# Kernel optimization log

Hardware: AMD Instinct MI355X
Metric: run time of the kernel (lower is better)

Reference implementation:

```python
import jax, jax.numpy as jnp
import numpy as np

EPS = 1e-5

def _bn(x, g, b, m, v):
    # eval-mode batchnorm, NCHW, per-channel params
    inv = g / jnp.sqrt(v + EPS)
    return x * inv[None, :, None, None] + (b - m * inv)[None, :, None, None]

def setup_inputs() -> dict:
    key = jax.random.key(0)
    ks = jax.random.split(key, 16)
    C = 64
    x = jax.random.normal(ks[0], (8, C, 64, 64), dtype=jnp.float32)
    w1 = jax.random.normal(ks[1], (C, C, 1, 1), dtype=jnp.float32) * 0.1
    w2 = jax.random.normal(ks[2], (C, 1, 3, 3), dtype=jnp.float32) * 0.1
    w3 = jax.random.normal(ks[3], (C, C, 1, 1), dtype=jnp.float32) * 0.1
    def bn_params(k):
        k1, k2, k3, k4 = jax.random.split(k, 4)
        return (jax.random.uniform(k1, (C,)) + 0.5,
                jax.random.normal(k2, (C,)) * 0.1,
                jax.random.normal(k3, (C,)) * 0.1,
                jax.random.uniform(k4, (C,)) + 0.5)
    g1, b1, m1, v1 = bn_params(ks[4])
    g2, b2, m2, v2 = bn_params(ks[5])
    g3, b3, m3, v3 = bn_params(ks[6])
    return {"x": x, "w1": w1, "bn1_g": g1, "bn1_b": b1, "bn1_m": m1, "bn1_v": v1,
            "w2": w2, "bn2_g": g2, "bn2_b": b2, "bn2_m": m2, "bn2_v": v2,
            "w3": w3, "bn3_g": g3, "bn3_b": b3, "bn3_m": m3, "bn3_v": v3}

def reference(x, w1, bn1_g, bn1_b, bn1_m, bn1_v,
              w2, bn2_g, bn2_b, bn2_m, bn2_v,
              w3, bn3_g, bn3_b, bn3_m, bn3_v):
    B, c, h, w = x.shape
    N = h * w
    # conv1 (1x1) + BN + ReLU -> V
    v = jnp.einsum('bchw,oc->bohw', x, w1[:, :, 0, 0])
    v = jax.nn.relu(_bn(v, bn1_g, bn1_b, bn1_m, bn1_v))
    # attention over spatial positions: Q=K=x, single head, dim=c
    Q = x.reshape(B, c, N)          # bdn
    V = v.reshape(B, c, N)          # bdm
    scores = jnp.einsum('bdn,bdm->bnm', Q, Q) / (c ** 0.5)  # [B,N,N]
    prob = jax.nn.softmax(scores, axis=-1)
    out = jnp.einsum('bnm,bdm->bdn', prob, V).reshape(B, c, h, w)
    # depthwise conv + BN + ReLU
    out = jax.lax.conv_general_dilated(
        out, w2, window_strides=(1, 1), padding='SAME',
        dimension_numbers=('NCHW', 'OIHW', 'NCHW'), feature_group_count=c)
    out = jax.nn.relu(_bn(out, bn2_g, bn2_b, bn2_m, bn2_v))
    # pointwise conv + BN
    out = jnp.einsum('bchw,oc->bohw', out, w3[:, :, 0, 0])
    out = _bn(out, bn3_g, bn3_b, bn3_m, bn3_v)
    # residual (stride==1 and in_size==out_size)
    return out + x
```

## Files before the change

kernel.cpp:

```cpp
#include <hip/hip_runtime.h>
#include <stdint.h>

typedef __attribute__((ext_vector_type(8)))  short s16x8;
typedef __attribute__((ext_vector_type(16))) float f32x16;
typedef __attribute__((ext_vector_type(2)))  unsigned u32x2;

union CvtI4 { int4 i; s16x8 s; };
union CvtU4 { uint4 u; s16x8 s; };

__device__ __forceinline__ unsigned f2bf(float f) {
    union { float f; unsigned u; } v; v.f = f;
    return (v.u + 0x7fffu + ((v.u >> 16) & 1u)) >> 16;
}

__device__ __forceinline__ unsigned packbf(float lo, float hi) {
    union { float f; unsigned u; } a0, a1;
    a0.f = lo; a1.f = hi;
    return __builtin_amdgcn_perm(a1.u + 0x8000u, a0.u + 0x8000u, 0x07060302u);
}

__global__ __launch_bounds__(256) void k_prep(
    const float* __restrict__ x, const float* __restrict__ w1,
    const float* __restrict__ g1, const float* __restrict__ b1,
    const float* __restrict__ m1, const float* __restrict__ v1,
    unsigned short* __restrict__ xT, unsigned short* __restrict__ vbf)
{
    __shared__ float X[64 * 65];
    const int b    = blockIdx.x >> 7;
    const int n0   = ((blockIdx.x >> 1) & 63) << 6;
    const int half = blockIdx.x & 1;
    const int tid  = threadIdx.x;
    const float QS = 0.42466090014400953f;

    {
        const int r = tid >> 6, nn = tid & 63;
        const float* xb = x + (size_t)b * 262144 + n0 + nn;
#pragma unroll
        for (int cc = 0; cc < 16; ++cc) {
            int c = cc * 4 + r;
            X[c * 65 + nn] = xb[(size_t)c * 4096];
        }
    }
    __syncthreads();

    {
        const int n8 = tid >> 3, c8 = tid & 7;
        const int n = (half << 5) + n8;
        unsigned u[4];
#pragma unroll
        for (int j = 0; j < 4; ++j) {
            unsigned lo = f2bf(X[(c8 * 8 + 2 * j) * 65 + n] * QS);
            unsigned hi = f2bf(X[(c8 * 8 + 2 * j + 1) * 65 + n] * QS);
            u[j] = lo | (hi << 16);
        }
        uint4 pk; pk.x = u[0]; pk.y = u[1]; pk.z = u[2]; pk.w = u[3];
        *(uint4*)(xT + (((size_t)((b << 12) + n0 + n)) << 6) + (c8 << 3)) = pk;
    }

    {
        const int n = tid & 63, og = tid >> 6;
        float rX[64];
#pragma unroll
        for (int c = 0; c < 64; ++c) rX[c] = X[c * 65 + n];
        unsigned short* vb = vbf + (((size_t)(b << 6)) << 12) + n0 + n;
#pragma unroll 2
        for (int oo = 0; oo < 8; ++oo) {
            int o = (half << 5) + og * 8 + oo;
            float inv = g1[o] * rsqrtf(v1[o] + 1e-5f);
            float sh  = b1[o] - m1[o] * inv;
            float acc = 0.f;
#pragma unroll
            for (int c = 0; c < 64; ++c) acc = fmaf(w1[o * 64 + c], rX[c], acc);
            vb[(size_t)o << 12] = (unsigned short)f2bf(fmaxf(fmaf(acc, inv, sh), 0.f));
        }
    }
}

__global__ __launch_bounds__(512, 4) void k_attn(
    const unsigned short* __restrict__ xT, const unsigned short* __restrict__ vbf,
    unsigned short* __restrict__ outO)
{
    __shared__ __align__(16) unsigned short Kl[2][2][64 * 64];
    __shared__ __align__(16) unsigned short Vl[2][2][64 * 64];

    const int b    = blockIdx.x & 7;
    const int qgrp = blockIdx.x >> 3;
    const int tid  = threadIdx.x;
    const int w = tid >> 6, lane = tid & 63;
    const int l31 = lane & 31, half = lane >> 5;
    const int qbase = qgrp << 6;
    const int qd = w & 3, par = w >> 2;
    const int s = qd & 1;
    const int t = qd >> 1;

    s16x8 Bq[4];
    {
        const unsigned short* qr = xT +
            (((size_t)((b << 12) + qbase + (t << 5) + l31)) << 6) + (half << 3);
#pragma unroll
        for (int kk = 0; kk < 4; ++kk) {
            CvtI4 c; c.i = *(const int4*)(qr + (kk << 4));
            Bq[kk] = c.s;
        }
    }

    const int pt = tid >> 8;
    const int sr = (tid >> 3) & 31;
    const int sc = tid & 7;
    const unsigned short* kBase = xT  + ((size_t)b << 18) + (sr << 6) + (sc << 3);
    const unsigned short* vBase = vbf + ((size_t)b << 18) + ((size_t)sr << 12) + (sc << 3);
    const int kx  = (sc ^ (sr & 7)) << 3;
    const int d0  = (sr << 6) + kx;
    const int d1  = ((sr + 32) << 6) + kx;

    int4 kpA, kpB, vpA, vpB;

    {
        int4 a0 = *(const int4*)(kBase + ((size_t)pt << 12));
        int4 a1 = *(const int4*)(kBase + ((size_t)pt << 12) + (32 << 6));
        int4 b0 = *(const int4*)(vBase + (pt << 6));
        int4 b1v = *(const int4*)(vBase + ((size_t)32 << 12) + (pt << 6));
        unsigned short* Kd = &Kl[0][pt][0];
        unsigned short* Vd = &Vl[0][pt][0];
        *(int4*)(Kd + d0) = a0; *(int4*)(Kd + d1) = a1;
        *(int4*)(Vd + d0) = b0; *(int4*)(Vd + d1) = b1v;
        const int t1 = 2 + pt;
        kpA = *(const int4*)(kBase + ((size_t)t1 << 12));
        kpB = *(const int4*)(kBase + ((size_t)t1 << 12) + (32 << 6));
        vpA = *(const int4*)(vBase + (t1 << 6));
        vpB = *(const int4*)(vBase + ((size_t)32 << 12) + (t1 << 6));
    }
    __syncthreads();

    f32x16 O[2];
#pragma unroll
    for (int dl = 0; dl < 2; ++dl)
#pragma unroll
        for (int r = 0; r < 16; ++r) O[dl][r] = 0.f;
    float rs = 0.f;

    const int km = (s << 5) + l31;

    for (int p = 0; p < 32; ++p) {
        {
            unsigned short* Kd = &Kl[(p + 1) & 1][pt][0];
            unsigned short* Vd = &Vl[(p + 1) & 1][pt][0];
            *(int4*)(Kd + d0) = kpA; *(int4*)(Kd + d1) = kpB;
            *(int4*)(Vd + d0) = vpA; *(int4*)(Vd + d1) = vpB;
        }
        {
            int tn = ((p + 2) << 1) + pt; if (tn > 63) tn = 63;
            kpA = *(const int4*)(kBase + ((size_t)tn << 12));
            kpB = *(const int4*)(kBase + ((size_t)tn << 12) + (32 << 6));
            vpA = *(const int4*)(vBase + (tn << 6));
            vpB = *(const int4*)(vBase + ((size_t)32 << 12) + (tn << 6));
        }

        const unsigned short* Kb = &Kl[p & 1][par][0];
        s16x8 Ak[4];
#pragma unroll
        for (int kk = 0; kk < 4; ++kk)
            Ak[kk] = *(const s16x8*)(Kb + (km << 6) + ((((kk << 1) + half) ^ (km & 7)) << 3));
        f32x16 S = {0.f,0.f,0.f,0.f,0.f,0.f,0.f,0.f,0.f,0.f,0.f,0.f,0.f,0.f,0.f,0.f};
        __builtin_amdgcn_s_setprio(1);
        S = __builtin_amdgcn_mfma_f32_32x32x16_bf16(Ak[0], Bq[0], S, 0, 0, 0);
        S = __builtin_amdgcn_mfma_f32_32x32x16_bf16(Ak[1], Bq[1], S, 0, 0, 0);
        S = __builtin_amdgcn_mfma_f32_32x32x16_bf16(Ak[2], Bq[2], S, 0, 0, 0);
        S = __builtin_amdgcn_mfma_f32_32x32x16_bf16(Ak[3], Bq[3], S, 0, 0, 0);
        __builtin_amdgcn_s_setprio(0);

        uint2 G[4];
#pragma unroll
        for (int q = 0; q < 4; ++q) {
            float p0 = __builtin_amdgcn_exp2f(S[4*q+0]);
            float p1 = __builtin_amdgcn_exp2f(S[4*q+1]);
            float p2 = __builtin_amdgcn_exp2f(S[4*q+2]);
            float p3 = __builtin_amdgcn_exp2f(S[4*q+3]);
            rs += (p0 + p1) + (p2 + p3);
            G[q].x = packbf(p0, p1);
            G[q].y = packbf(p2, p3);
        }

        const unsigned short* Vb = &Vl[p & 1][par][0];
        __builtin_amdgcn_s_setprio(1);
#pragma unroll
        for (int ksl = 0; ksl < 2; ++ksl) {
            u32x2 r0 = __builtin_amdgcn_permlane32_swap(G[2*ksl].x, G[2*ksl+1].x, false, false);
            u32x2 r1 = __builtin_amdgcn_permlane32_swap(G[2*ksl].y, G[2*ksl+1].y, false, false);
            CvtU4 ac;
            ac.u.x = r0.x;
            ac.u.y = r1.x;
            ac.u.z = r0.y;
            ac.u.w = r1.y;
            const s16x8 Ap = ac.s;
#pragma unroll
            for (int dl = 0; dl < 2; ++dl) {
                const int drow = (dl << 5) + l31;
                const int cch = (s << 2) + (ksl << 1) + half;
                const s16x8 Bv = *(const s16x8*)(Vb + (drow << 6) + ((cch ^ (drow & 7)) << 3));
                O[dl] = __builtin_amdgcn_mfma_f32_32x32x16_bf16(Ap, Bv, O[dl], 0, 0, 0);
            }
        }
        __builtin_amdgcn_s_setprio(0);

        __syncthreads();
    }

    float* scr  = (float*)&Kl[0][0][0];
    float* scr2 = (float*)&Vl[0][0][0];
    float* rsL  = scr2 + 4096;
    float* dnm  = rsL + 256;

    rs += __shfl_xor(rs, 32);
    if (half == 0) rsL[(w << 5) + l31] = rs;
    if (par == 1) {
#pragma unroll
        for (int dl = 0; dl < 2; ++dl)
#pragma unroll
            for (int r = 0; r < 16; ++r)
                scr[((((qd << 1) + dl)) << 10) + (r << 6) + lane] = O[dl][r];
    }
    __syncthreads();

    if (tid < 64) {
        int tt = tid >> 5, n = tid & 31;
        dnm[tid] = (rsL[((tt << 1) << 5) + n] + rsL[(((tt << 1) + 1) << 5) + n]) +
                   (rsL[(((tt << 1) + 4) << 5) + n] + rsL[(((tt << 1) + 5) << 5) + n]);
    }
    if (par == 0) {
#pragma unroll
        for (int dl = 0; dl < 2; ++dl)
#pragma unroll
            for (int r = 0; r < 16; ++r)
                O[dl][r] += scr[((((qd << 1) + dl)) << 10) + (r << 6) + lane];
        if (s == 1) {
#pragma unroll
            for (int dl = 0; dl < 2; ++dl)
#pragma unroll
                for (int r = 0; r < 16; ++r)
                    scr2[((((t << 1) + dl)) << 10) + (r << 6) + lane] = O[dl][r];
        }
    }
    __syncthreads();

    if (par == 0 && s == 0) {
        const int nb = (b << 12) + qbase;
#pragma unroll
        for (int r = 0; r < 16; ++r) {
            int rowoff = (r & 3) + ((r >> 2) << 3) + (half << 2);
            int n = (t << 5) + rowoff;
            float inv = 1.f / dnm[n];
#pragma unroll
            for (int dl = 0; dl < 2; ++dl) {
                float o = O[dl][r] + scr2[((((t << 1) + dl)) << 10) + (r << 6) + lane];
                outO[((size_t)(nb + n) << 6) + (dl << 5) + l31] =
                    (unsigned short)f2bf(o * inv);
            }
        }
    }
}

__global__ __launch_bounds__(256) void k_post(
    const unsigned short* __restrict__ Obase,
    const float* __restrict__ x,
    const float* __restrict__ w2,
    const float* __restrict__ g2, const float* __restrict__ b2,
    const float* __restrict__ m2, const float* __restrict__ v2,
    const float* __restrict__ w3,
    const float* __restrict__ g3, const float* __restrict__ b3,
    const float* __restrict__ m3, const float* __restrict__ v3,
    float* __restrict__ out)
{
    __shared__ float W[3][34 * 66];
    __shared__ float T2[32 * 66];

    const int b  = blockIdx.x >> 7;
    const int h  = (blockIdx.x >> 1) & 63;
    const int wh = blockIdx.x & 1;
    const int wbase = wh << 5;
    const int tid = threadIdx.x;

#pragma unroll
    for (int r = 0; r < 3; ++r) {
        int hh = h + r - 1;
#pragma unroll
        for (int i = 0; i < 2; ++i) {
            int lin = (i << 8) + tid;
            if (lin < 272) {
                int wl = lin >> 3, cg = lin & 7;
                int wg = wbase + wl - 1;
                float* Wd = &W[r][wl * 66 + (cg << 3)];
                if (hh >= 0 && hh <= 63 && wg >= 0 && wg <= 63) {
                    size_t npos = (size_t)((b << 12) + (hh << 6) + wg);
                    uint4 v = *(const uint4*)(Obase + (npos << 6) + (cg << 3));
                    union { float f; unsigned u; } t;
                    t.u = v.x << 16;         Wd[0] = t.f;
                    t.u = v.x & 0xFFFF0000u; Wd[1] = t.f;
                    t.u = v.y << 16;         Wd[2] = t.f;
                    t.u = v.y & 0xFFFF0000u; Wd[3] = t.f;
                    t.u = v.z << 16;         Wd[4] = t.f;
                    t.u = v.z & 0xFFFF0000u; Wd[5] = t.f;
                    t.u = v.w << 16;         Wd[6] = t.f;
                    t.u = v.w & 0xFFFF0000u; Wd[7] = t.f;
                } else {
#pragma unroll
                    for (int j = 0; j < 8; ++j) Wd[j] = 0.f;
                }
            }
        }
    }
    __syncthreads();

    const int w32 = tid & 31, cq = tid >> 5;
    float t8[8];
#pragma unroll
    for (int i = 0; i < 8; ++i) t8[i] = 0.f;

#pragma unroll
    for (int ky = 0; ky < 3; ++ky) {
#pragma unroll
        for (int kx = 0; kx < 3; ++kx) {
            const int k = ky * 3 + kx;
            const float* Wr = &W[ky][(w32 + kx) * 66 + (cq << 3)];
#pragma unroll
            for (int i = 0; i < 2; ++i) {
                float4 a = *(const float4*)(Wr + (i << 2));
                int c = (cq << 3) + (i << 2);
                t8[i * 4 + 0] = fmaf(w2[(c + 0) * 9 + k], a.x, t8[i * 4 + 0]);
                t8[i * 4 + 1] = fmaf(w2[(c + 1) * 9 + k], a.y, t8[i * 4 + 1]);
                t8[i * 4 + 2] = fmaf(w2[(c + 2) * 9 + k], a.z, t8[i * 4 + 2]);
                t8[i * 4 + 3] = fmaf(w2[(c + 3) * 9 + k], a.w, t8[i * 4 + 3]);
            }
        }
    }
#pragma unroll
    for (int i = 0; i < 8; ++i) {
        int c = (cq << 3) + i;
        float inv = g2[c] * rsqrtf(v2[c] + 1e-5f);
        float sh  = b2[c] - m2[c] * inv;
        T2[w32 * 66 + c] = fmaxf(fmaf(t8[i], inv, sh), 0.f);
    }
    __syncthreads();

    float rT[64];
#pragma unroll
    for (int c4 = 0; c4 < 16; ++c4)
        *(float4*)&rT[c4 << 2] = *(const float4*)&T2[w32 * 66 + (c4 << 2)];

    const int hw = (h << 6) + wbase + w32;
#pragma unroll 2
    for (int oo = 0; oo < 8; ++oo) {
        int o = (cq << 3) + oo;
        float inv = g3[o] * rsqrtf(v3[o] + 1e-5f);
        float sh  = b3[o] - m3[o] * inv;
        float acc = 0.f;
#pragma unroll
        for (int c = 0; c < 64; ++c) acc = fmaf(w3[o * 64 + c], rT[c], acc);
        size_t idx = (((size_t)((b << 6) + o)) << 12) + hw;
        out[idx] = fmaf(acc, inv, sh) + x[idx];
    }
}

extern "C" void kernel_launch(void* const* d_in, const int* in_sizes, int n_in,
                              void* d_out, int out_size, void* d_ws, size_t ws_size,
                              hipStream_t stream)
{
    const float* x  = (const float*)d_in[0];
    const float* w1 = (const float*)d_in[1];
    const float* g1 = (const float*)d_in[2];
    const float* b1 = (const float*)d_in[3];
    const float* m1 = (const float*)d_in[4];
    const float* v1 = (const float*)d_in[5];
    const float* w2 = (const float*)d_in[6];
    const float* g2 = (const float*)d_in[7];
    const float* b2 = (const float*)d_in[8];
    const float* m2 = (const float*)d_in[9];
    const float* v2 = (const float*)d_in[10];
    const float* w3 = (const float*)d_in[11];
    const float* g3 = (const float*)d_in[12];
    const float* b3 = (const float*)d_in[13];
    const float* m3 = (const float*)d_in[14];
    const float* v3 = (const float*)d_in[15];
    float* out = (float*)d_out;

    unsigned short* xT  = (unsigned short*)d_ws;
    unsigned short* vbf = xT + (size_t)8 * 4096 * 64;
    unsigned short* Obase = (unsigned short*)((char*)d_ws + (8u << 20));

    k_prep<<<1024, 256, 0, stream>>>(x, w1, g1, b1, m1, v1, xT, vbf);
    k_attn<<<512, 512, 0, stream>>>(xT, vbf, Obase);
    k_post<<<1024, 256, 0, stream>>>(Obase, x, w2, g2, b2, m2, v2,
                                     w3, g3, b3, m3, v3, out);
}
```

Measured before the change: 184.8 us.

## Double query tile per attention block to reuse K/V tiles across two query groups

Result: no change. 184.7 us (-0.1%).

```diff
diff --git a/kernel.cpp b/kernel.cpp
--- a/kernel.cpp
+++ b/kernel.cpp
@@ -76,31 +76,34 @@
     }
 }
 
-__global__ __launch_bounds__(512, 4) void k_attn(
+__global__ __launch_bounds__(512, 2) void k_attn(
     const unsigned short* __restrict__ xT, const unsigned short* __restrict__ vbf,
     unsigned short* __restrict__ outO)
 {
     __shared__ __align__(16) unsigned short Kl[2][2][64 * 64];
     __shared__ __align__(16) unsigned short Vl[2][2][64 * 64];
-
-    const int b    = blockIdx.x & 7;
-    const int qgrp = blockIdx.x >> 3;
-    const int tid  = threadIdx.x;
+    __shared__ float rsL[8][2][32];
+    __shared__ float dnm[128];
+
+    const int b   = blockIdx.x & 7;
+    const int qg2 = blockIdx.x >> 3;
+    const int tid = threadIdx.x;
     const int w = tid >> 6, lane = tid & 63;
     const int l31 = lane & 31, half = lane >> 5;
-    const int qbase = qgrp << 6;
+    const int qbase = qg2 << 7;
     const int qd = w & 3, par = w >> 2;
     const int s = qd & 1;
     const int t = qd >> 1;
 
-    s16x8 Bq[4];
-    {
+    s16x8 Bq[2][4];
+#pragma unroll
+    for (int ti = 0; ti < 2; ++ti) {
         const unsigned short* qr = xT +
-            (((size_t)((b << 12) + qbase + (t << 5) + l31)) << 6) + (half << 3);
+            (((size_t)((b << 12) + qbase + ((t + 2 * ti) << 5) + l31)) << 6) + (half << 3);
 #pragma unroll
         for (int kk = 0; kk < 4; ++kk) {
             CvtI4 c; c.i = *(const int4*)(qr + (kk << 4));
-            Bq[kk] = c.s;
+            Bq[ti][kk] = c.s;
         }
     }
 
@@ -132,12 +135,14 @@
     }
     __syncthreads();
 
-    f32x16 O[2];
-#pragma unroll
-    for (int dl = 0; dl < 2; ++dl)
-#pragma unroll
-        for (int r = 0; r < 16; ++r) O[dl][r] = 0.f;
-    float rs = 0.f;
+    f32x16 O[2][2];
+#pragma unroll
+    for (int ti = 0; ti < 2; ++ti)
+#pragma unroll
+        for (int dl = 0; dl < 2; ++dl)
+#pragma unroll
+            for (int r = 0; r < 16; ++r) O[ti][dl][r] = 0.f;
+    float rs[2] = {0.f, 0.f};
 
     const int km = (s << 5) + l31;
 
@@ -161,44 +166,50 @@
 #pragma unroll
         for (int kk = 0; kk < 4; ++kk)
             Ak[kk] = *(const s16x8*)(Kb + (km << 6) + ((((kk << 1) + half) ^ (km & 7)) << 3));
-        f32x16 S = {0.f,0.f,0.f,0.f,0.f,0.f,0.f,0.f,0.f,0.f,0.f,0.f,0.f,0.f,0.f,0.f};
-        __builtin_amdgcn_s_setprio(1);
-        S = __builtin_amdgcn_mfma_f32_32x32x16_bf16(Ak[0], Bq[0], S, 0, 0, 0);
-        S = __builtin_amdgcn_mfma_f32_32x32x16_bf16(Ak[1], Bq[1], S, 0, 0, 0);
-        S = __builtin_amdgcn_mfma_f32_32x32x16_bf16(Ak[2], Bq[2], S, 0, 0, 0);
-        S = __builtin_amdgcn_mfma_f32_32x32x16_bf16(Ak[3], Bq[3], S, 0, 0, 0);
-        __builtin_amdgcn_s_setprio(0);
-
-        uint2 G[4];
-#pragma unroll
-        for (int q = 0; q < 4; ++q) {
-            float p0 = __builtin_amdgcn_exp2f(S[4*q+0]);
-            float p1 = __builtin_amdgcn_exp2f(S[4*q+1]);
-            float p2 = __builtin_amdgcn_exp2f(S[4*q+2]);
-            float p3 = __builtin_amdgcn_exp2f(S[4*q+3]);
-            rs += (p0 + p1) + (p2 + p3);
-            G[q].x = packbf(p0, p1);
-            G[q].y = packbf(p2, p3);
+
+        uint2 G[2][4];
+#pragma unroll
+        for (int ti = 0; ti < 2; ++ti) {
+            f32x16 S = {0.f,0.f,0.f,0.f,0.f,0.f,0.f,0.f,0.f,0.f,0.f,0.f,0.f,0.f,0.f,0.f};
+            __builtin_amdgcn_s_setprio(1);
+            S = __builtin_amdgcn_mfma_f32_32x32x16_bf16(Ak[0], Bq[ti][0], S, 0, 0, 0);
+            S = __builtin_amdgcn_mfma_f32_32x32x16_bf16(Ak[1], Bq[ti][1], S, 0, 0, 0);
+            S = __builtin_amdgcn_mfma_f32_32x32x16_bf16(Ak[2], Bq[ti][2], S, 0, 0, 0);
+            S = __builtin_amdgcn_mfma_f32_32x32x16_bf16(Ak[3], Bq[ti][3], S, 0, 0, 0);
+            __builtin_amdgcn_s_setprio(0);
+#pragma unroll
+            for (int q = 0; q < 4; ++q) {
+                float p0 = __builtin_amdgcn_exp2f(S[4*q+0]);
+                float p1 = __builtin_amdgcn_exp2f(S[4*q+1]);
+                float p2 = __builtin_amdgcn_exp2f(S[4*q+2]);
+                float p3 = __builtin_amdgcn_exp2f(S[4*q+3]);
+                rs[ti] += (p0 + p1) + (p2 + p3);
+                G[ti][q].x = packbf(p0, p1);
+                G[ti][q].y = packbf(p2, p3);
+            }
         }
 
         const unsigned short* Vb = &Vl[p & 1][par][0];
         __builtin_amdgcn_s_setprio(1);
 #pragma unroll
         for (int ksl = 0; ksl < 2; ++ksl) {
-            u32x2 r0 = __builtin_amdgcn_permlane32_swap(G[2*ksl].x, G[2*ksl+1].x, false, false);
-            u32x2 r1 = __builtin_amdgcn_permlane32_swap(G[2*ksl].y, G[2*ksl+1].y, false, false);
-            CvtU4 ac;
-            ac.u.x = r0.x;
-            ac.u.y = r1.x;
-            ac.u.z = r0.y;
-            ac.u.w = r1.y;
-            const s16x8 Ap = ac.s;
-#pragma unroll
-            for (int dl = 0; dl < 2; ++dl) {
-                const int drow = (dl << 5) + l31;
-                const int cch = (s << 2) + (ksl << 1) + half;
-                const s16x8 Bv = *(const s16x8*)(Vb + (drow << 6) + ((cch ^ (drow & 7)) << 3));
-                O[dl] = __builtin_amdgcn_mfma_f32_32x32x16_bf16(Ap, Bv, O[dl], 0, 0, 0);
+            const int cch = (s << 2) + (ksl << 1) + half;
+            const int dr0 = l31;
+            const int dr1 = 32 + l31;
+            const s16x8 Bv0 = *(const s16x8*)(Vb + (dr0 << 6) + ((cch ^ (dr0 & 7)) << 3));
+            const s16x8 Bv1 = *(const s16x8*)(Vb + (dr1 << 6) + ((cch ^ (dr1 & 7)) << 3));
+#pragma unroll
+            for (int ti = 0; ti < 2; ++ti) {
+                u32x2 r0 = __builtin_amdgcn_permlane32_swap(G[ti][2*ksl].x, G[ti][2*ksl+1].x, false, false);
+                u32x2 r1 = __builtin_amdgcn_permlane32_swap(G[ti][2*ksl].y, G[ti][2*ksl+1].y, false, false);
+                CvtU4 ac;
+                ac.u.x = r0.x;
+                ac.u.y = r1.x;
+                ac.u.z = r0.y;
+                ac.u.w = r1.y;
+                const s16x8 Ap = ac.s;
+                O[ti][0] = __builtin_amdgcn_mfma_f32_32x32x16_bf16(Ap, Bv0, O[ti][0], 0, 0, 0);
+                O[ti][1] = __builtin_amdgcn_mfma_f32_32x32x16_bf16(Ap, Bv1, O[ti][1], 0, 0, 0);
             }
         }
         __builtin_amdgcn_s_setprio(0);
@@ -206,57 +217,71 @@
         __syncthreads();
     }
 
-    float* scr  = (float*)&Kl[0][0][0];
-    float* scr2 = (float*)&Vl[0][0][0];
-    float* rsL  = scr2 + 4096;
-    float* dnm  = rsL + 256;
-
-    rs += __shfl_xor(rs, 32);
-    if (half == 0) rsL[(w << 5) + l31] = rs;
+    float* scrK = (float*)&Kl[0][0][0];
+    float* scrV = (float*)&Vl[0][0][0];
+
+    rs[0] += __shfl_xor(rs[0], 32);
+    rs[1] += __shfl_xor(rs[1], 32);
+    if (half == 0) { rsL[w][0][l31] = rs[0]; rsL[w][1][l31] = rs[1]; }
+
     if (par == 1) {
-#pragma unroll
-        for (int dl = 0; dl < 2; ++dl)
-#pragma unroll
-            for (int r = 0; r < 16; ++r)
-                scr[((((qd << 1) + dl)) << 10) + (r << 6) + lane] = O[dl][r];
-    }
-    __syncthreads();
-
-    if (tid < 64) {
-        int tt = tid >> 5, n = tid & 31;
-        dnm[tid] = (rsL[((tt << 1) << 5) + n] + rsL[(((tt << 1) + 1) << 5) + n]) +
-                   (rsL[(((tt << 1) + 4) << 5) + n] + rsL[(((tt << 1) + 5) << 5) + n]);
+        float* rg = (qd < 2) ? scrK : scrV;
+        const int q1 = qd & 1;
+#pragma unroll
+        for (int ti = 0; ti < 2; ++ti)
+#pragma unroll
+            for (int dl = 0; dl < 2; ++dl)
+#pragma unroll
+                for (int r = 0; r < 16; ++r)
+                    rg[(((q1 << 2) + (ti << 1) + dl) << 10) + (r << 6) + lane] = O[ti][dl][r];
+    }
+    __syncthreads();
+
+    if (tid < 128) {
+        int tp = tid >> 5, n32 = tid & 31;
+        int ti = tp >> 1, tl = tp & 1;
+        dnm[tid] = (rsL[(tl << 1) + 0][ti][n32] + rsL[(tl << 1) + 1][ti][n32]) +
+                   (rsL[(tl << 1) + 4][ti][n32] + rsL[(tl << 1) + 5][ti][n32]);
     }
     if (par == 0) {
-#pragma unroll
-        for (int dl = 0; dl < 2; ++dl)
-#pragma unroll
-            for (int r = 0; r < 16; ++r)
-                O[dl][r] += scr[((((qd << 1) + dl)) << 10) + (r << 6) + lane];
-        if (s == 1) {
+        float* rg = (qd < 2) ? scrK : scrV;
+        const int q1 = qd & 1;
+#pragma unroll
+        for (int ti = 0; ti < 2; ++ti)
 #pragma unroll
             for (int dl = 0; dl < 2; ++dl)
 #pragma unroll
                 for (int r = 0; r < 16; ++r)
-                    scr2[((((t << 1) + dl)) << 10) + (r << 6) + lane] = O[dl][r];
-        }
+                    O[ti][dl][r] += rg[(((q1 << 2) + (ti << 1) + dl) << 10) + (r << 6) + lane];
+    }
+    __syncthreads();
+
+    if (par == 0 && s == 1) {
+#pragma unroll
+        for (int ti = 0; ti < 2; ++ti)
+#pragma unroll
+            for (int dl = 0; dl < 2; ++dl)
+#pragma unroll
+                for (int r = 0; r < 16; ++r)
+                    scrK[(((t << 2) + (ti << 1) + dl) << 10) + (r << 6) + lane] = O[ti][dl][r];
     }
     __syncthreads();
 
     if (par == 0 && s == 0) {
         const int nb = (b << 12) + qbase;
 #pragma unroll
-        for (int r = 0; r < 16; ++r) {
-            int rowoff = (r & 3) + ((r >> 2) << 3) + (half << 2);
-            int n = (t << 5) + rowoff;
-            float inv = 1.f / dnm[n];
-#pragma unroll
-            for (int dl = 0; dl < 2; ++dl) {
-                float o = O[dl][r] + scr2[((((t << 1) + dl)) << 10) + (r << 6) + lane];
-                outO[((size_t)(nb + n) << 6) + (dl << 5) + l31] =
-                    (unsigned short)f2bf(o * inv);
-            }
-        }
+        for (int ti = 0; ti < 2; ++ti)
+#pragma unroll
+            for (int dl = 0; dl < 2; ++dl)
+#pragma unroll
+                for (int r = 0; r < 16; ++r) {
+                    int rowoff = (r & 3) + ((r >> 2) << 3) + (half << 2);
+                    int n = ((t + 2 * ti) << 5) + rowoff;
+                    float o = O[ti][dl][r] +
+                              scrK[(((t << 2) + (ti << 1) + dl) << 10) + (r << 6) + lane];
+                    outO[((size_t)(nb + n) << 6) + (dl << 5) + l31] =
+                        (unsigned short)f2bf(o * (1.f / dnm[n]));
+                }
     }
 }
 
@@ -388,7 +413,7 @@
     unsigned short* Obase = (unsigned short*)((char*)d_ws + (8u << 20));
 
     k_prep<<<1024, 256, 0, stream>>>(x, w1, g1, b1, m1, v1, xT, vbf);
-    k_attn<<<512, 512, 0, stream>>>(xT, vbf, Obase);
+    k_attn<<<256, 512, 0, stream>>>(xT, vbf, Obase);
     k_post<<<1024, 256, 0, stream>>>(Obase, x, w2, g2, b2, m2, v2,
                                      w3, g3, b3, m3, v3, out);
 }
```

## Double attention block to 128 queries and software-pipeline PV MFMA behind QK

Applied to the files above, without the earlier changes.

Result: no change. 184.1 us (-0.4%).

```diff
diff --git a/kernel.cpp b/kernel.cpp
--- a/kernel.cpp
+++ b/kernel.cpp
@@ -76,27 +76,29 @@
     }
 }
 
-__global__ __launch_bounds__(512, 4) void k_attn(
+__global__ __launch_bounds__(1024, 4) void k_attn(
     const unsigned short* __restrict__ xT, const unsigned short* __restrict__ vbf,
     unsigned short* __restrict__ outO)
 {
     __shared__ __align__(16) unsigned short Kl[2][2][64 * 64];
     __shared__ __align__(16) unsigned short Vl[2][2][64 * 64];
-
-    const int b    = blockIdx.x & 7;
-    const int qgrp = blockIdx.x >> 3;
-    const int tid  = threadIdx.x;
+    __shared__ float rsL[16][32];
+    __shared__ float dnm[128];
+
+    const int b   = blockIdx.x & 7;
+    const int qg2 = blockIdx.x >> 3;
+    const int tid = threadIdx.x;
     const int w = tid >> 6, lane = tid & 63;
     const int l31 = lane & 31, half = lane >> 5;
-    const int qbase = qgrp << 6;
-    const int qd = w & 3, par = w >> 2;
-    const int s = qd & 1;
-    const int t = qd >> 1;
+    const int qbase = qg2 << 7;
+    const int qd = w & 7, par = w >> 3;
+    const int s  = qd & 1;
+    const int t2 = qd >> 1;
 
     s16x8 Bq[4];
     {
         const unsigned short* qr = xT +
-            (((size_t)((b << 12) + qbase + (t << 5) + l31)) << 6) + (half << 3);
+            (((size_t)((b << 12) + qbase + (t2 << 5) + l31)) << 6) + (half << 3);
 #pragma unroll
         for (int kk = 0; kk < 4; ++kk) {
             CvtI4 c; c.i = *(const int4*)(qr + (kk << 4));
@@ -104,31 +106,24 @@
         }
     }
 
-    const int pt = tid >> 8;
-    const int sr = (tid >> 3) & 31;
-    const int sc = tid & 7;
+    const int pt = tid >> 9;
+    const int u  = tid & 511;
+    const int sr = u >> 3;
+    const int sc = u & 7;
     const unsigned short* kBase = xT  + ((size_t)b << 18) + (sr << 6) + (sc << 3);
     const unsigned short* vBase = vbf + ((size_t)b << 18) + ((size_t)sr << 12) + (sc << 3);
-    const int kx  = (sc ^ (sr & 7)) << 3;
-    const int d0  = (sr << 6) + kx;
-    const int d1  = ((sr + 32) << 6) + kx;
-
-    int4 kpA, kpB, vpA, vpB;
+    const int d = (sr << 6) + ((sc ^ (sr & 7)) << 3);
+
+    int4 kp, vp;
 
     {
         int4 a0 = *(const int4*)(kBase + ((size_t)pt << 12));
-        int4 a1 = *(const int4*)(kBase + ((size_t)pt << 12) + (32 << 6));
         int4 b0 = *(const int4*)(vBase + (pt << 6));
-        int4 b1v = *(const int4*)(vBase + ((size_t)32 << 12) + (pt << 6));
-        unsigned short* Kd = &Kl[0][pt][0];
-        unsigned short* Vd = &Vl[0][pt][0];
-        *(int4*)(Kd + d0) = a0; *(int4*)(Kd + d1) = a1;
-        *(int4*)(Vd + d0) = b0; *(int4*)(Vd + d1) = b1v;
+        *(int4*)(&Kl[0][pt][0] + d) = a0;
+        *(int4*)(&Vl[0][pt][0] + d) = b0;
         const int t1 = 2 + pt;
-        kpA = *(const int4*)(kBase + ((size_t)t1 << 12));
-        kpB = *(const int4*)(kBase + ((size_t)t1 << 12) + (32 << 6));
-        vpA = *(const int4*)(vBase + (t1 << 6));
-        vpB = *(const int4*)(vBase + ((size_t)32 << 12) + (t1 << 6));
+        kp = *(const int4*)(kBase + ((size_t)t1 << 12));
+        vp = *(const int4*)(vBase + (t1 << 6));
     }
     __syncthreads();
 
@@ -139,21 +134,25 @@
         for (int r = 0; r < 16; ++r) O[dl][r] = 0.f;
     float rs = 0.f;
 
+    uint2 Gh[4];
+    s16x8 Bvh[4];
+    {
+        const s16x8 z = {0, 0, 0, 0, 0, 0, 0, 0};
+#pragma unroll
+        for (int q = 0; q < 4; ++q) { Gh[q].x = 0u; Gh[q].y = 0u; }
+#pragma unroll
+        for (int j = 0; j < 4; ++j) Bvh[j] = z;
+    }
+
     const int km = (s << 5) + l31;
 
     for (int p = 0; p < 32; ++p) {
         {
-            unsigned short* Kd = &Kl[(p + 1) & 1][pt][0];
-            unsigned short* Vd = &Vl[(p + 1) & 1][pt][0];
-            *(int4*)(Kd + d0) = kpA; *(int4*)(Kd + d1) = kpB;
-            *(int4*)(Vd + d0) = vpA; *(int4*)(Vd + d1) = vpB;
-        }
-        {
+            *(int4*)(&Kl[(p + 1) & 1][pt][0] + d) = kp;
+            *(int4*)(&Vl[(p + 1) & 1][pt][0] + d) = vp;
             int tn = ((p + 2) << 1) + pt; if (tn > 63) tn = 63;
-            kpA = *(const int4*)(kBase + ((size_t)tn << 12));
-            kpB = *(const int4*)(kBase + ((size_t)tn << 12) + (32 << 6));
-            vpA = *(const int4*)(vBase + (tn << 6));
-            vpB = *(const int4*)(vBase + ((size_t)32 << 12) + (tn << 6));
+            kp = *(const int4*)(kBase + ((size_t)tn << 12));
+            vp = *(const int4*)(vBase + (tn << 6));
         }
 
         const unsigned short* Kb = &Kl[p & 1][par][0];
@@ -161,15 +160,26 @@
 #pragma unroll
         for (int kk = 0; kk < 4; ++kk)
             Ak[kk] = *(const s16x8*)(Kb + (km << 6) + ((((kk << 1) + half) ^ (km & 7)) << 3));
+
+        __builtin_amdgcn_s_setprio(1);
+#pragma unroll
+        for (int ksl = 0; ksl < 2; ++ksl) {
+            u32x2 r0 = __builtin_amdgcn_permlane32_swap(Gh[2*ksl].x, Gh[2*ksl+1].x, false, false);
+            u32x2 r1 = __builtin_amdgcn_permlane32_swap(Gh[2*ksl].y, Gh[2*ksl+1].y, false, false);
+            CvtU4 ac;
+            ac.u.x = r0.x; ac.u.y = r1.x; ac.u.z = r0.y; ac.u.w = r1.y;
+            const s16x8 Ap = ac.s;
+            O[0] = __builtin_amdgcn_mfma_f32_32x32x16_bf16(Ap, Bvh[2*ksl + 0], O[0], 0, 0, 0);
+            O[1] = __builtin_amdgcn_mfma_f32_32x32x16_bf16(Ap, Bvh[2*ksl + 1], O[1], 0, 0, 0);
+        }
+
         f32x16 S = {0.f,0.f,0.f,0.f,0.f,0.f,0.f,0.f,0.f,0.f,0.f,0.f,0.f,0.f,0.f,0.f};
-        __builtin_amdgcn_s_setprio(1);
         S = __builtin_amdgcn_mfma_f32_32x32x16_bf16(Ak[0], Bq[0], S, 0, 0, 0);
         S = __builtin_amdgcn_mfma_f32_32x32x16_bf16(Ak[1], Bq[1], S, 0, 0, 0);
         S = __builtin_amdgcn_mfma_f32_32x32x16_bf16(Ak[2], Bq[2], S, 0, 0, 0);
         S = __builtin_amdgcn_mfma_f32_32x32x16_bf16(Ak[3], Bq[3], S, 0, 0, 0);
         __builtin_amdgcn_s_setprio(0);
 
-        uint2 G[4];
 #pragma unroll
         for (int q = 0; q < 4; ++q) {
             float p0 = __builtin_amdgcn_exp2f(S[4*q+0]);
@@ -177,86 +187,89 @@
             float p2 = __builtin_amdgcn_exp2f(S[4*q+2]);
             float p3 = __builtin_amdgcn_exp2f(S[4*q+3]);
             rs += (p0 + p1) + (p2 + p3);
-            G[q].x = packbf(p0, p1);
-            G[q].y = packbf(p2, p3);
-        }
-
-        const unsigned short* Vb = &Vl[p & 1][par][0];
-        __builtin_amdgcn_s_setprio(1);
-#pragma unroll
-        for (int ksl = 0; ksl < 2; ++ksl) {
-            u32x2 r0 = __builtin_amdgcn_permlane32_swap(G[2*ksl].x, G[2*ksl+1].x, false, false);
-            u32x2 r1 = __builtin_amdgcn_permlane32_swap(G[2*ksl].y, G[2*ksl+1].y, false, false);
-            CvtU4 ac;
-            ac.u.x = r0.x;
-            ac.u.y = r1.x;
-            ac.u.z = r0.y;
-            ac.u.w = r1.y;
-            const s16x8 Ap = ac.s;
-#pragma unroll
-            for (int dl = 0; dl < 2; ++dl) {
-                const int drow = (dl << 5) + l31;
-                const int cch = (s << 2) + (ksl << 1) + half;
-                const s16x8 Bv = *(const s16x8*)(Vb + (drow << 6) + ((cch ^ (drow & 7)) << 3));
-                O[dl] = __builtin_amdgcn_mfma_f32_32x32x16_bf16(Ap, Bv, O[dl], 0, 0, 0);
-            }
-        }
-        __builtin_amdgcn_s_setprio(0);
+            Gh[q].x = packbf(p0, p1);
+            Gh[q].y = packbf(p2, p3);
+        }
+
+        {
+            const unsigned short* Vb = &Vl[p & 1][par][0];
+#pragma unroll
+            for (int ksl = 0; ksl < 2; ++ksl)
+#pragma unroll
+                for (int dl = 0; dl < 2; ++dl) {
+                    const int drow = (dl << 5) + l31;
+                    const int cch = (s << 2) + (ksl << 1) + half;
+                    Bvh[2*ksl + dl] =
+                        *(const s16x8*)(Vb + (drow << 6) + ((cch ^ (drow & 7)) << 3));
+                }
+        }
 
         __syncthreads();
     }
 
-    float* scr  = (float*)&Kl[0][0][0];
-    float* scr2 = (float*)&Vl[0][0][0];
-    float* rsL  = scr2 + 4096;
-    float* dnm  = rsL + 256;
+#pragma unroll
+    for (int ksl = 0; ksl < 2; ++ksl) {
+        u32x2 r0 = __builtin_amdgcn_permlane32_swap(Gh[2*ksl].x, Gh[2*ksl+1].x, false, false);
+        u32x2 r1 = __builtin_amdgcn_permlane32_swap(Gh[2*ksl].y, Gh[2*ksl+1].y, false, false);
+        CvtU4 ac;
+        ac.u.x = r0.x; ac.u.y = r1.x; ac.u.z = r0.y; ac.u.w = r1.y;
+        const s16x8 Ap = ac.s;
+        O[0] = __builtin_amdgcn_mfma_f32_32x32x16_bf16(Ap, Bvh[2*ksl + 0], O[0], 0, 0, 0);
+        O[1] = __builtin_amdgcn_mfma_f32_32x32x16_bf16(Ap, Bvh[2*ksl + 1], O[1], 0, 0, 0);
+    }
+
+    float* scrK = (float*)&Kl[0][0][0];
+    float* scrV = (float*)&Vl[0][0][0];
 
     rs += __shfl_xor(rs, 32);
-    if (half == 0) rsL[(w << 5) + l31] = rs;
+    if (half == 0) rsL[w][l31] = rs;
+
     if (par == 1) {
+        float* rg = (qd < 4) ? (scrK + (qd << 11)) : (scrV + ((qd - 4) << 11));
 #pragma unroll
         for (int dl = 0; dl < 2; ++dl)
 #pragma unroll
             for (int r = 0; r < 16; ++r)
-                scr[((((qd << 1) + dl)) << 10) + (r << 6) + lane] = O[dl][r];
-    }
-    __syncthreads();
-
-    if (tid < 64) {
-        int tt = tid >> 5, n = tid & 31;
-        dnm[tid] = (rsL[((tt << 1) << 5) + n] + rsL[(((tt << 1) + 1) << 5) + n]) +
-                   (rsL[(((tt << 1) + 4) << 5) + n] + rsL[(((tt << 1) + 5) << 5) + n]);
+                rg[(dl << 10) + (r << 6) + lane] = O[dl][r];
+    }
+    __syncthreads();
+
+    if (tid < 128) {
+        int tt = tid >> 5, n32 = tid & 31;
+        dnm[tid] = (rsL[(tt << 1) + 0][n32] + rsL[(tt << 1) + 1][n32]) +
+                   (rsL[(tt << 1) + 8][n32] + rsL[(tt << 1) + 9][n32]);
     }
     if (par == 0) {
+        float* rg = (qd < 4) ? (scrK + (qd << 11)) : (scrV + ((qd - 4) << 11));
 #pragma unroll
         for (int dl = 0; dl < 2; ++dl)
 #pragma unroll
             for (int r = 0; r < 16; ++r)
-                O[dl][r] += scr[((((qd << 1) + dl)) << 10) + (r << 6) + lane];
-        if (s == 1) {
-#pragma unroll
-            for (int dl = 0; dl < 2; ++dl)
-#pragma unroll
-                for (int r = 0; r < 16; ++r)
-                    scr2[((((t << 1) + dl)) << 10) + (r << 6) + lane] = O[dl][r];
-        }
+                O[dl][r] += rg[(dl << 10) + (r << 6) + lane];
+    }
+    __syncthreads();
+
+    if (par == 0 && s == 1) {
+#pragma unroll
+        for (int dl = 0; dl < 2; ++dl)
+#pragma unroll
+            for (int r = 0; r < 16; ++r)
+                scrK[(t2 << 11) + (dl << 10) + (r << 6) + lane] = O[dl][r];
     }
     __syncthreads();
 
     if (par == 0 && s == 0) {
         const int nb = (b << 12) + qbase;
 #pragma unroll
-        for (int r = 0; r < 16; ++r) {
-            int rowoff = (r & 3) + ((r >> 2) << 3) + (half << 2);
-            int n = (t << 5) + rowoff;
-            float inv = 1.f / dnm[n];
-#pragma unroll
-            for (int dl = 0; dl < 2; ++dl) {
-                float o = O[dl][r] + scr2[((((t << 1) + dl)) << 10) + (r << 6) + lane];
+        for (int dl = 0; dl < 2; ++dl)
+#pragma unroll
+            for (int r = 0; r < 16; ++r) {
+                int rowoff = (r & 3) + ((r >> 2) << 3) + (half << 2);
+                int n = (t2 << 5) + rowoff;
+                float o = O[dl][r] + scrK[(t2 << 11) + (dl << 10) + (r << 6) + lane];
                 outO[((size_t)(nb + n) << 6) + (dl << 5) + l31] =
-                    (unsigned short)f2bf(o * inv);
+                    (unsigned short)f2bf(o * (1.f / dnm[n]));
             }
-        }
     }
 }
 
@@ -388,7 +401,7 @@
     unsigned short* Obase = (unsigned short*)((char*)d_ws + (8u << 20));
 
     k_prep<<<1024, 256, 0, stream>>>(x, w1, g1, b1, m1, v1, xT, vbf);
-    k_attn<<<512, 512, 0, stream>>>(xT, vbf, Obase);
+    k_attn<<<256, 1024, 0, stream>>>(xT, vbf, Obase);
     k_post<<<1024, 256, 0, stream>>>(Obase, x, w2, g2, b2, m2, v2,
                                      w3, g3, b3, m3, v3, out);
 }
```
